# Performance work log

Measured on AMD Instinct MI355X. Metric: run time of the kernel, lower is better.

Reference implementation:

```python
import jax, jax.numpy as jnp
import numpy as np

B, N, C, H = 2, 2048, 1024, 16
D = C // H
EPS = 1e-5  # torch LayerNorm default


def layernorm(x, gamma, beta):
    mu = jnp.mean(x, axis=-1, keepdims=True)
    var = jnp.mean(jnp.square(x - mu), axis=-1, keepdims=True)
    return (x - mu) * jax.lax.rsqrt(var + EPS) * gamma + beta


def setup_inputs() -> dict:
    key = jax.random.key(0)
    ks = jax.random.split(key, 4)
    x = jax.random.normal(ks[0], (B, N, C), dtype=jnp.float32)
    w_qkv = jax.random.normal(ks[1], (3 * C, C), dtype=jnp.float32) * (C ** -0.5)
    w_proj = jax.random.normal(ks[2], (C, C), dtype=jnp.float32) * (C ** -0.5)
    return {
        "x": x,
        "w_qkv": w_qkv,
        "q_gamma": jnp.ones((C,), jnp.float32),
        "q_beta": jnp.zeros((C,), jnp.float32),
        "k_gamma": jnp.ones((C,), jnp.float32),
        "k_beta": jnp.zeros((C,), jnp.float32),
        "lpe_w": jnp.ones((C,), jnp.float32),
        "lpe_b": jnp.zeros((C,), jnp.float32),
        "w_proj": w_proj,
        "b_proj": jnp.zeros((C,), jnp.float32),
    }


def reference(x, w_qkv, q_gamma, q_beta, k_gamma, k_beta, lpe_w, lpe_b, w_proj, b_proj):
    b, n, c = x.shape
    scale = D ** -0.5
    qkv = jnp.einsum('bnc,fc->bnf', x, w_qkv)            # (B,N,3C)
    qkv = qkv.reshape(b, n, 3, H, D)
    q, k, v = qkv[:, :, 0], qkv[:, :, 1], qkv[:, :, 2]   # (B,N,H,D)
    # QK-norm: LayerNorm over flattened heads (dim C)
    q = layernorm(q.reshape(b, n, c), q_gamma, q_beta).reshape(b, n, H, D)
    k = layernorm(k.reshape(b, n, c), k_gamma, k_beta).reshape(b, n, H, D)
    # LPE: depthwise 1x1x1 conv == per-channel affine on v
    v_lpe = v.reshape(b, n, c) * lpe_w + lpe_b           # (B,N,C)
    # attention
    attn = jnp.einsum('bqhd,bkhd->bhqk', q * scale, k)   # (B,H,N,N)
    attn = jax.nn.softmax(attn, axis=-1)
    out = jnp.einsum('bhqk,bkhd->bqhd', attn, v).reshape(b, n, c)
    y = jnp.einsum('bnc,oc->bno', out + v_lpe, w_proj) + b_proj
    return y
```

## Files before the change

### kernel.cpp

```cpp
#include <hip/hip_runtime.h>
#include <stdint.h>

#define Bdim 2
#define Ndim 2048
#define Cdim 1024
#define Hdim 16
#define Ddim 64
#define Fdim 3072
#define Mdim 4096

typedef unsigned int  u32;
typedef unsigned short u16;
typedef float f32x4 __attribute__((ext_vector_type(4)));
typedef short s16x8 __attribute__((ext_vector_type(8)));
typedef unsigned short u16x4 __attribute__((ext_vector_type(4)));
typedef unsigned int u32x2 __attribute__((ext_vector_type(2)));

__device__ __forceinline__ u16 f2b(float f) {
  u32 u = __builtin_bit_cast(u32, f);
  u += 0x7FFFu + ((u >> 16) & 1u);
  return (u16)(u >> 16);
}
__device__ __forceinline__ float b2f(u16 h) {
  return __builtin_bit_cast(float, (u32)h << 16);
}
__device__ __forceinline__ u32 cvtpk(float a, float b) {
  u32 d;
  asm("v_cvt_pk_bf16_f32 %0, %1, %2" : "=v"(d) : "v"(a), "v"(b));
  return d;
}
__device__ __forceinline__ float rexp2(float x) { return __builtin_amdgcn_exp2f(x); }
__device__ __forceinline__ f32x4 mfma16(s16x8 a, s16x8 b, f32x4 c) {
  return __builtin_amdgcn_mfma_f32_16x16x32_bf16(a, b, c, 0, 0, 0);
}
__device__ __forceinline__ void gl_lds16(const void* g, void* l) {
  __builtin_amdgcn_global_load_lds(
      (const __attribute__((address_space(1))) void*)g,
      (__attribute__((address_space(3))) void*)l, 16, 0, 0);
}
__device__ __forceinline__ bool is_bf16(const void* qg) {
  return *(const u32*)qg == 0x3F803F80u;
}

__global__ __launch_bounds__(256)
void k_prep(const void* x, const void* wq, const void* wp,
            const void* g0, const void* g1, const void* g2, const void* g3,
            const void* g4, const void* g5, const void* g6,
            u16* xb, u16* wqb, u16* wpb, float* prm) {
  const int i = blockIdx.x * 256 + threadIdx.x;
  const bool isbf = is_bf16(g0);
  const void* src; u16* dst; int k;
  if (i < 1048576)      { src = x;  dst = xb;  k = i; }
  else if (i < 1835008) { src = wq; dst = wqb; k = i - 1048576; }
  else if (i < 2097152) { src = wp; dst = wpb; k = i - 1835008; }
  else {
    const int j = i - 2097152;
    if (j >= 1792) return;
    const int fi = j * 4;
    const int pi = fi >> 10, off = fi & 1023;
    const void* s = (pi == 0) ? g0 : (pi == 1) ? g1 : (pi == 2) ? g2
                  : (pi == 3) ? g3 : (pi == 4) ? g4 : (pi == 5) ? g5 : g6;
    float4 v;
    if (isbf) {
      u16x4 h = *(const u16x4*)((const u16*)s + off);
      v.x = b2f(h.x); v.y = b2f(h.y); v.z = b2f(h.z); v.w = b2f(h.w);
    } else {
      v = *(const float4*)((const float*)s + off);
    }
    *(float4*)(prm + fi) = v;
    return;
  }
  if (isbf) {
    ((u16x4*)dst)[k] = ((const u16x4*)src)[k];
  } else {
    float4 v = ((const float4*)src)[k];
    u16x4 o;
    o.x = f2b(v.x); o.y = f2b(v.y); o.z = f2b(v.z); o.w = f2b(v.w);
    ((u16x4*)dst)[k] = o;
  }
}

template <int EPI>
__global__ __launch_bounds__(256)
void k_gemm_bt(const u16* __restrict__ A, const u16* __restrict__ W,
               u16* __restrict__ Cb, void* __restrict__ Cout,
               u16* __restrict__ vTp,
               const float* __restrict__ bias, const void* __restrict__ qg,
               int Msz, int Nsz, int Ksz) {
  __shared__ __align__(16) char lds[32768];
  const int tid = threadIdx.x;
  const int lane = tid & 63;
  const int wm = (tid >> 6) >> 1, wn = (tid >> 6) & 1;
  const int g = lane >> 4, cl = lane & 15;
  const int nwg = gridDim.x * gridDim.y;
  const int lid = blockIdx.y * gridDim.x + blockIdx.x;
  const int cpx = nwg >> 3;
  const int swz = (lid & 7) * cpx + (lid >> 3);
  const int row0 = (swz / gridDim.x) * 128, col0 = (swz % gridDim.x) * 128;
  const int KT = Ksz >> 5;

  f32x4 acc[4][4] = {};

  auto stage = [&](int buf, int kt) {
    const int k0 = kt << 5;
#pragma unroll
    for (int iss = 0; iss < 2; ++iss) {
      const int t = iss * 256 + tid;
      const int r = t >> 2;
      const int ss = (t & 3) ^ ((r >> 1) & 3);
      gl_lds16(A + (size_t)(row0 + r) * Ksz + k0 + ss * 8, &lds[buf * 16384 + t * 16]);
      gl_lds16(W + (size_t)(col0 + r) * Ksz + k0 + ss * 8, &lds[buf * 16384 + 8192 + t * 16]);
    }
  };

  stage(0, 0);
  __syncthreads();
  int cur = 0;
  for (int kt = 0; kt < KT; ++kt) {
    if (kt + 1 < KT) stage(cur ^ 1, kt + 1);
    const char* Ab = &lds[cur * 16384];
    const char* Bb = &lds[cur * 16384 + 8192];
    s16x8 af[4], bfr[4];
#pragma unroll
    for (int mi = 0; mi < 4; ++mi) {
      const int r = wm * 64 + mi * 16 + cl;
      const int s = g ^ ((r >> 1) & 3);
      af[mi] = *(const s16x8*)(Ab + r * 64 + s * 16);
    }
#pragma unroll
    for (int nj = 0; nj < 4; ++nj) {
      const int r = wn * 64 + nj * 16 + cl;
      const int s = g ^ ((r >> 1) & 3);
      bfr[nj] = *(const s16x8*)(Bb + r * 64 + s * 16);
    }
#pragma unroll
    for (int mi = 0; mi < 4; ++mi)
#pragma unroll
      for (int nj = 0; nj < 4; ++nj)
        acc[mi][nj] = mfma16(af[mi], bfr[nj], acc[mi][nj]);
    __syncthreads();
    cur ^= 1;
  }

  const u32 oflag = (EPI == 1) ? (is_bf16(qg) ? 1u : 0u) : 0u;
#pragma unroll
  for (int mi = 0; mi < 4; ++mi)
#pragma unroll
    for (int nj = 0; nj < 4; ++nj) {
      const int m0 = row0 + wm * 64 + mi * 16 + g * 4;
      const int nbase = col0 + wn * 64 + nj * 16;
      const int n = nbase + cl;
      if (EPI == 2 && nbase >= 2048) {
        const int h = (nbase - 2048) >> 6;
        const int d = ((nbase - 2048) & 63) + cl;
        u16x4 pk;
#pragma unroll
        for (int r = 0; r < 4; ++r) pk[r] = f2b(acc[mi][nj][r]);
        *(u16x4*)(vTp + (size_t)h * (64 * 4096) + (size_t)d * 4096 + m0) = pk;
      } else {
#pragma unroll
        for (int r = 0; r < 4; ++r) {
          const int m = m0 + r;
          float v = acc[mi][nj][r];
          if (EPI == 2) {
            Cb[(size_t)m * Nsz + n] = f2b(v);
          } else {
            v += bias[n];
            if (oflag) ((u16*)Cout)[(size_t)m * Nsz + n] = f2b(v);
            else       ((float*)Cout)[(size_t)m * Nsz + n] = v;
          }
        }
      }
    }
}

__global__ __launch_bounds__(256)
void k_ln(u16* __restrict__ qkv, const float* __restrict__ prm) {
  const int m = blockIdx.x;
  const int tid = threadIdx.x;
  const int lane = tid & 63, wv = tid >> 6;
  __shared__ float red[2][4];
  u16* row = qkv + (size_t)m * Fdim;
#pragma unroll
  for (int seg = 0; seg < 2; ++seg) {
    u16* s = row + seg * 1024;
    u16x4 v = *(const u16x4*)(s + tid * 4);
    float x0 = b2f(v.x), x1 = b2f(v.y), x2 = b2f(v.z), x3 = b2f(v.w);
    float sum = x0 + x1 + x2 + x3;
    float ssq = x0 * x0 + x1 * x1 + x2 * x2 + x3 * x3;
#pragma unroll
    for (int off = 32; off >= 1; off >>= 1) {
      sum += __shfl_xor(sum, off);
      ssq += __shfl_xor(ssq, off);
    }
    if (lane == 0) { red[0][wv] = sum; red[1][wv] = ssq; }
    __syncthreads();
    const float ts = red[0][0] + red[0][1] + red[0][2] + red[0][3];
    const float tq = red[1][0] + red[1][1] + red[1][2] + red[1][3];
    __syncthreads();
    const float mu = ts * (1.0f / 1024.0f);
    const float var = tq * (1.0f / 1024.0f) - mu * mu;
    const float rstd = rsqrtf(var + 1e-5f);
    const float scl = (seg == 0) ? (0.125f * 1.4426950408889634f) : 1.0f;
    const float* gam = prm + seg * 2048;
    const float* bet = prm + seg * 2048 + 1024;
    const int c = tid * 4;
    u16x4 o;
    o.x = f2b(((x0 - mu) * rstd * gam[c + 0] + bet[c + 0]) * scl);
    o.y = f2b(((x1 - mu) * rstd * gam[c + 1] + bet[c + 1]) * scl);
    o.z = f2b(((x2 - mu) * rstd * gam[c + 2] + bet[c + 2]) * scl);
    o.w = f2b(((x3 - mu) * rstd * gam[c + 3] + bet[c + 3]) * scl);
    *(u16x4*)(s + tid * 4) = o;
  }
}

__global__ __launch_bounds__(256, 3)
void k_attn(const u16* __restrict__ qkv, const u16* __restrict__ vT,
            u16* __restrict__ pin, const float* __restrict__ prm) {
  const int bid = blockIdx.x;
  const int qt = (bid >> 3) & 15;
  const int bh = (bid & 7) * 4 + (bid >> 7);
  const int b = bh >> 4, h = bh & 15;
  const int tid = threadIdx.x, lane = tid & 63, w = tid >> 6;
  const int g = lane >> 4, cl = lane & 15;
  const int c7 = cl & 7;
  const int mrow0 = b * Ndim + qt * 128;
  const int NT = Ndim / 64;

  const u16* Qg  = qkv + (size_t)mrow0 * Fdim + h * 64;
  const u16* Kg  = qkv + (size_t)(b * Ndim) * Fdim + Cdim + h * 64;
  const u16* vTg = vT + (size_t)h * (64 * 4096) + b * Ndim;

  __shared__ __align__(16) char klds[2][8192];
  __shared__ __align__(16) char vlds[2][8192];
  __shared__ __align__(16) char plds[4][4096];

  s16x8 bq[2][2];
#pragma unroll
  for (int qb = 0; qb < 2; ++qb)
#pragma unroll
    for (int kc = 0; kc < 2; ++kc)
      bq[qb][kc] = *(const s16x8*)(Qg + (size_t)(w * 32 + qb * 16 + cl) * Fdim + kc * 32 + g * 8);

  f32x4 o[2][4] = {};
  float mr[2] = {-1e30f, -1e30f};
  float lr[2] = {0.f, 0.f};

  const char* akp0 = &klds[0][cl * 128 + (((0 + g) ^ c7) << 4)];
  const char* akp1 = &klds[0][cl * 128 + (((4 + g) ^ c7) << 4)];
  const char* avp0 = &vlds[0][cl * 128 + (((0 + g) ^ c7) << 4)];
  const char* avp1 = &vlds[0][cl * 128 + (((4 + g) ^ c7) << 4)];
  char* pwp[4];
#pragma unroll
  for (int nj = 0; nj < 4; ++nj)
    pwp[nj] = &plds[w][cl * 128 + ((nj * 32 + g * 8) ^ (c7 << 4))];
  const char* bpp0 = &plds[w][cl * 128 + ((0  + g * 16) ^ (c7 << 4))];
  const char* bpp1 = &plds[w][cl * 128 + ((64 + g * 16) ^ (c7 << 4))];

  const int r0 = tid >> 3;
  const int ss0 = ((tid & 7) ^ (r0 & 7)) * 8;
  const u16* kp = Kg + (size_t)r0 * Fdim + ss0;
  const u16* vp = vTg + (size_t)r0 * 4096 + ss0;
  char* kd = &klds[0][tid * 16];
  char* vd = &vlds[0][tid * 16];

  gl_lds16(kp, kd);
  gl_lds16(kp + (size_t)32 * Fdim, kd + 4096);
  gl_lds16(vp, vd);
  gl_lds16(vp + (size_t)32 * 4096, vd + 4096);
  kp += (size_t)64 * Fdim;
  vp += 64;

#define ATTN_TILE(BUF, PREFETCH)                                              \
  {                                                                           \
               \
    asm volatile("s_waitcnt vmcnt(2)" ::: "memory");                          \
    __builtin_amdgcn_s_barrier();                                             \
    __builtin_amdgcn_sched_barrier(0);                                        \
    if (PREFETCH) {                                                           \
      gl_lds16(kp, kd + ((BUF) ^ 1) * 8192);                                  \
      gl_lds16(kp + (size_t)32 * Fdim, kd + ((BUF) ^ 1) * 8192 + 4096);       \
      gl_lds16(vp, vd + ((BUF) ^ 1) * 8192);                                  \
      gl_lds16(vp + (size_t)32 * 4096, vd + ((BUF) ^ 1) * 8192 + 4096);       \
      kp += (size_t)64 * Fdim;                                                \
      vp += 64;                                                               \
    }                                                                         \
    s16x8 ak[4][2];                                                           \
    _Pragma("unroll") for (int nj = 0; nj < 4; ++nj) {                        \
      ak[nj][0] = *(const s16x8*)(akp0 + (BUF) * 8192 + nj * 2048);           \
      ak[nj][1] = *(const s16x8*)(akp1 + (BUF) * 8192 + nj * 2048);           \
    }                                                                         \
    _Pragma("unroll") for (int qb = 0; qb < 2; ++qb) {                        \
      f32x4 sv[4];                                                            \
      __builtin_amdgcn_s_setprio(1);                                          \
      _Pragma("unroll") for (int nj = 0; nj < 4; ++nj) {                      \
        f32x4 z = {0.f, 0.f, 0.f, 0.f};                                       \
        z = mfma16(ak[nj][0], bq[qb][0], z);                                  \
        z = mfma16(ak[nj][1], bq[qb][1], z);                                  \
        sv[nj] = z;                                                           \
      }                                                                       \
      __builtin_amdgcn_s_setprio(0);                                          \
      float a0 = fmaxf(fmaxf(sv[0][0], sv[0][1]), sv[0][2]);                  \
      float a1 = fmaxf(fmaxf(sv[0][3], sv[1][0]), sv[1][1]);                  \
      float a2 = fmaxf(fmaxf(sv[1][2], sv[1][3]), sv[2][0]);                  \
      float a3 = fmaxf(fmaxf(sv[2][1], sv[2][2]), sv[2][3]);                  \
      float a4 = fmaxf(fmaxf(sv[3][0], sv[3][1]), sv[3][2]);                  \
      float b0v = fmaxf(fmaxf(a0, a1), a2);                                   \
      float b1v = fmaxf(fmaxf(a3, a4), sv[3][3]);                             \
      float mx = fmaxf(b0v, b1v);                                             \
      if (!__all(mx <= mr[qb] + 7.0f)) {                                      \
        mx = fmaxf(mx, __shfl_xor(mx, 16));                                   \
        mx = fmaxf(mx, __shfl_xor(mx, 32));                                   \
        const float mn = fmaxf(mr[qb], mx);                                   \
        const float corr = rexp2(mr[qb] - mn);                                \
        mr[qb] = mn;                                                          \
        lr[qb] *= corr;                                                       \
        o[qb][0] *= corr; o[qb][1] *= corr;                                   \
        o[qb][2] *= corr; o[qb][3] *= corr;                                   \
      }                                                                       \
      const float mrq = mr[qb];                                               \
      float ssum = 0.f;                                                       \
      _Pragma("unroll") for (int nj = 0; nj < 4; ++nj) {                      \
        const float p0 = rexp2(sv[nj][0] - mrq), p1 = rexp2(sv[nj][1] - mrq); \
        const float p2 = rexp2(sv[nj][2] - mrq), p3 = rexp2(sv[nj][3] - mrq); \
        ssum += (p0 + p1) + (p2 + p3);                                        \
        u32x2 pk2;                                                            \
        pk2.x = cvtpk(p0, p1);                                                \
        pk2.y = cvtpk(p2, p3);                                                \
        *(u32x2*)(pwp[nj] + qb * 2048) = pk2;                                 \
      }                                                                       \
      lr[qb] += ssum;                                                         \
    }                                                                         \
           \
    if (PREFETCH) {                                                           \
      asm volatile("s_waitcnt vmcnt(4) lgkmcnt(0)" ::: "memory");             \
    } else {                                                                  \
      asm volatile("s_waitcnt vmcnt(0) lgkmcnt(0)" ::: "memory");             \
    }                                                                         \
    __builtin_amdgcn_s_barrier();                                             \
    __builtin_amdgcn_sched_barrier(0);                                        \
    s16x8 av[4][2];                                                           \
    _Pragma("unroll") for (int dc = 0; dc < 4; ++dc) {                        \
      av[dc][0] = *(const s16x8*)(avp0 + (BUF) * 8192 + dc * 2048);           \
      av[dc][1] = *(const s16x8*)(avp1 + (BUF) * 8192 + dc * 2048);           \
    }                                                                         \
    _Pragma("unroll") for (int qb = 0; qb < 2; ++qb) {                        \
      const s16x8 bp0 = *(const s16x8*)(bpp0 + qb * 2048);                    \
      const s16x8 bp1 = *(const s16x8*)(bpp1 + qb * 2048);                    \
      __builtin_amdgcn_s_setprio(1);                                          \
      _Pragma("unroll") for (int dc = 0; dc < 4; ++dc) {                      \
        o[qb][dc] = mfma16(av[dc][0], bp0, o[qb][dc]);                        \
        o[qb][dc] = mfma16(av[dc][1], bp1, o[qb][dc]);                        \
      }                                                                       \
      __builtin_amdgcn_s_setprio(0);                                          \
    }                                                                         \
  }

  for (int t = 0; t < NT; t += 2) {
    ATTN_TILE(0, true);
    ATTN_TILE(1, (t + 2 < NT));
  }
#undef ATTN_TILE

#pragma unroll
  for (int qb = 0; qb < 2; ++qb) {
    const int q = w * 32 + qb * 16 + cl;
    const int m = mrow0 + q;
    const int nseq = qt * 128 + q;
    float lt = lr[qb];
    lt += __shfl_xor(lt, 16);
    lt += __shfl_xor(lt, 32);
    const float inv = 1.0f / lt;
#pragma unroll
    for (int dc = 0; dc < 4; ++dc) {
      const int d0 = dc * 16 + g * 4;
      const int c = h * 64 + d0;
      const float4 lw = *(const float4*)(prm + 4096 + c);
      const float4 lb = *(const float4*)(prm + 5120 + c);
      float vr[4];
#pragma unroll
      for (int r = 0; r < 4; ++r) {
        const float vv = b2f(vTg[(size_t)(d0 + r) * 4096 + nseq]);
        vr[r] = o[qb][dc][r] * inv + vv * (&lw.x)[r] + (&lb.x)[r];
      }
      u32x2 ov;
      ov.x = cvtpk(vr[0], vr[1]);
      ov.y = cvtpk(vr[2], vr[3]);
      *(u32x2*)(pin + (size_t)m * Cdim + c) = ov;
    }
  }
}

extern "C" void kernel_launch(void* const* d_in, const int* in_sizes, int n_in,
                              void* d_out, int out_size, void* d_ws, size_t ws_size,
                              hipStream_t stream) {
  (void)in_sizes; (void)n_in; (void)out_size; (void)ws_size;
  char* ws = (char*)d_ws;
  float* prm    = (float*)(ws + 256);
  u16*   xb     = (u16*)(ws + 32768);
  u16*   wqkvb  = (u16*)(ws + 32768 + 8388608);
  u16*   wprojb = (u16*)(ws + 32768 + 8388608 + 6291456);
  u16*   qkv    = (u16*)(ws + 32768 + 8388608 + 6291456 + 2097152);
  u16*   vT     = (u16*)(ws + 32768 + 8388608 + 6291456 + 2097152 + 25165824);
  u16*   pin    = xb;

  k_prep<<<8199, 256, 0, stream>>>(d_in[0], d_in[1], d_in[8],
                                   d_in[2], d_in[3], d_in[4], d_in[5],
                                   d_in[6], d_in[7], d_in[9],
                                   xb, wqkvb, wprojb, prm);

  k_gemm_bt<2><<<dim3(Fdim / 128, Mdim / 128), 256, 0, stream>>>(
      xb, wqkvb, qkv, nullptr, vT, nullptr, nullptr, Mdim, Fdim, Cdim);

  k_ln<<<Mdim, 256, 0, stream>>>(qkv, prm);

  k_attn<<<dim3(512), 256, 0, stream>>>(qkv, vT, pin, prm);

  k_gemm_bt<1><<<dim3(Cdim / 128, Mdim / 128), 256, 0, stream>>>(
      pin, wprojb, nullptr, d_out, nullptr, prm + 6144, d_in[2], Mdim, Cdim, Cdim);
}
```

Before: 133.2 us.

## Use 128x64 tiles for output projection GEMM and batch QK MFMAs in attention

The output projection GEMM moves from a 128x128 tile kernel (256 workgroups) to a dedicated 128x64 tile kernel, which doubles the workgroup count to 512 so the 256 CUs are better filled. The QKV GEMM becomes its own non-templated kernel. In attention, the QK^T MFMAs for both query blocks are now issued together under raised priority before the softmax work, so more matrix ops can be in flight. The smaller tile reloads the A operand twice as often and lowers per-wave reuse, and holding both score blocks at once raises register pressure in the attention kernel.

```diff
diff --git a/kernel.cpp b/kernel.cpp
--- a/kernel.cpp
+++ b/kernel.cpp
@@ -80,13 +80,10 @@
   }
 }
 
-template <int EPI>
 __global__ __launch_bounds__(256)
-void k_gemm_bt(const u16* __restrict__ A, const u16* __restrict__ W,
-               u16* __restrict__ Cb, void* __restrict__ Cout,
-               u16* __restrict__ vTp,
-               const float* __restrict__ bias, const void* __restrict__ qg,
-               int Msz, int Nsz, int Ksz) {
+void k_gemm_qkv(const u16* __restrict__ A, const u16* __restrict__ W,
+                u16* __restrict__ Cb, u16* __restrict__ vTp,
+                int Msz, int Nsz, int Ksz) {
   __shared__ __align__(16) char lds[32768];
   const int tid = threadIdx.x;
   const int lane = tid & 63;
@@ -142,7 +139,6 @@
     cur ^= 1;
   }
 
-  const u32 oflag = (EPI == 1) ? (is_bf16(qg) ? 1u : 0u) : 0u;
 #pragma unroll
   for (int mi = 0; mi < 4; ++mi)
 #pragma unroll
@@ -150,7 +146,7 @@
       const int m0 = row0 + wm * 64 + mi * 16 + g * 4;
       const int nbase = col0 + wn * 64 + nj * 16;
       const int n = nbase + cl;
-      if (EPI == 2 && nbase >= 2048) {
+      if (nbase >= 2048) {
         const int h = (nbase - 2048) >> 6;
         const int d = ((nbase - 2048) & 63) + cl;
         u16x4 pk;
@@ -159,17 +155,87 @@
         *(u16x4*)(vTp + (size_t)h * (64 * 4096) + (size_t)d * 4096 + m0) = pk;
       } else {
 #pragma unroll
-        for (int r = 0; r < 4; ++r) {
-          const int m = m0 + r;
-          float v = acc[mi][nj][r];
-          if (EPI == 2) {
-            Cb[(size_t)m * Nsz + n] = f2b(v);
-          } else {
-            v += bias[n];
-            if (oflag) ((u16*)Cout)[(size_t)m * Nsz + n] = f2b(v);
-            else       ((float*)Cout)[(size_t)m * Nsz + n] = v;
-          }
-        }
+        for (int r = 0; r < 4; ++r)
+          Cb[(size_t)(m0 + r) * Nsz + n] = f2b(acc[mi][nj][r]);
+      }
+    }
+}
+
+__global__ __launch_bounds__(256)
+void k_gemm_n64(const u16* __restrict__ A, const u16* __restrict__ W,
+                void* __restrict__ Cout, const float* __restrict__ bias,
+                const void* __restrict__ qg) {
+  __shared__ __align__(16) char lds[24576];
+  const int tid = threadIdx.x;
+  const int lane = tid & 63;
+  const int w = tid >> 6;
+  const int g = lane >> 4, cl = lane & 15;
+  const int nwg = gridDim.x * gridDim.y;
+  const int lid = blockIdx.y * gridDim.x + blockIdx.x;
+  const int cpx = nwg >> 3;
+  const int swz = (lid & 7) * cpx + (lid >> 3);
+  const int row0 = (swz / gridDim.x) * 128, col0 = (swz % gridDim.x) * 64;
+  const int KT = Cdim >> 5;
+
+  f32x4 acc[2][4] = {};
+
+  auto stage = [&](int buf, int kt) {
+    const int k0 = kt << 5;
+#pragma unroll
+    for (int iss = 0; iss < 2; ++iss) {
+      const int t = iss * 256 + tid;
+      const int r = t >> 2;
+      const int ss = (t & 3) ^ ((r >> 1) & 3);
+      gl_lds16(A + (size_t)(row0 + r) * Cdim + k0 + ss * 8, &lds[buf * 12288 + t * 16]);
+    }
+    {
+      const int r = tid >> 2;
+      const int ss = (tid & 3) ^ ((r >> 1) & 3);
+      gl_lds16(W + (size_t)(col0 + r) * Cdim + k0 + ss * 8, &lds[buf * 12288 + 8192 + tid * 16]);
+    }
+  };
+
+  stage(0, 0);
+  __syncthreads();
+  int cur = 0;
+  for (int kt = 0; kt < KT; ++kt) {
+    if (kt + 1 < KT) stage(cur ^ 1, kt + 1);
+    const char* Ab = &lds[cur * 12288];
+    const char* Bb = &lds[cur * 12288 + 8192];
+    s16x8 af[2], bfr[4];
+#pragma unroll
+    for (int mi = 0; mi < 2; ++mi) {
+      const int r = w * 32 + mi * 16 + cl;
+      const int s = g ^ ((r >> 1) & 3);
+      af[mi] = *(const s16x8*)(Ab + r * 64 + s * 16);
+    }
+#pragma unroll
+    for (int nj = 0; nj < 4; ++nj) {
+      const int r = nj * 16 + cl;
+      const int s = g ^ ((r >> 1) & 3);
+      bfr[nj] = *(const s16x8*)(Bb + r * 64 + s * 16);
+    }
+#pragma unroll
+    for (int mi = 0; mi < 2; ++mi)
+#pragma unroll
+      for (int nj = 0; nj < 4; ++nj)
+        acc[mi][nj] = mfma16(af[mi], bfr[nj], acc[mi][nj]);
+    __syncthreads();
+    cur ^= 1;
+  }
+
+  const u32 oflag = is_bf16(qg) ? 1u : 0u;
+#pragma unroll
+  for (int mi = 0; mi < 2; ++mi)
+#pragma unroll
+    for (int nj = 0; nj < 4; ++nj) {
+      const int m0 = row0 + w * 32 + mi * 16 + g * 4;
+      const int n = col0 + nj * 16 + cl;
+#pragma unroll
+      for (int r = 0; r < 4; ++r) {
+        float v = acc[mi][nj][r] + bias[n];
+        if (oflag) ((u16*)Cout)[(size_t)(m0 + r) * Cdim + n] = f2b(v);
+        else       ((float*)Cout)[(size_t)(m0 + r) * Cdim + n] = v;
       }
     }
 }
@@ -290,23 +356,25 @@
       ak[nj][0] = *(const s16x8*)(akp0 + (BUF) * 8192 + nj * 2048);           \
       ak[nj][1] = *(const s16x8*)(akp1 + (BUF) * 8192 + nj * 2048);           \
     }                                                                         \
-    _Pragma("unroll") for (int qb = 0; qb < 2; ++qb) {                        \
-      f32x4 sv[4];                                                            \
-      __builtin_amdgcn_s_setprio(1);                                          \
+                       \
+    f32x4 sv[2][4];                                                           \
+    __builtin_amdgcn_s_setprio(1);                                            \
+    _Pragma("unroll") for (int qb = 0; qb < 2; ++qb)                          \
       _Pragma("unroll") for (int nj = 0; nj < 4; ++nj) {                      \
         f32x4 z = {0.f, 0.f, 0.f, 0.f};                                       \
         z = mfma16(ak[nj][0], bq[qb][0], z);                                  \
         z = mfma16(ak[nj][1], bq[qb][1], z);                                  \
-        sv[nj] = z;                                                           \
+        sv[qb][nj] = z;                                                       \
       }                                                                       \
-      __builtin_amdgcn_s_setprio(0);                                          \
-      float a0 = fmaxf(fmaxf(sv[0][0], sv[0][1]), sv[0][2]);                  \
-      float a1 = fmaxf(fmaxf(sv[0][3], sv[1][0]), sv[1][1]);                  \
-      float a2 = fmaxf(fmaxf(sv[1][2], sv[1][3]), sv[2][0]);                  \
-      float a3 = fmaxf(fmaxf(sv[2][1], sv[2][2]), sv[2][3]);                  \
-      float a4 = fmaxf(fmaxf(sv[3][0], sv[3][1]), sv[3][2]);                  \
+    __builtin_amdgcn_s_setprio(0);                                            \
+    _Pragma("unroll") for (int qb = 0; qb < 2; ++qb) {                        \
+      float a0 = fmaxf(fmaxf(sv[qb][0][0], sv[qb][0][1]), sv[qb][0][2]);      \
+      float a1 = fmaxf(fmaxf(sv[qb][0][3], sv[qb][1][0]), sv[qb][1][1]);      \
+      float a2 = fmaxf(fmaxf(sv[qb][1][2], sv[qb][1][3]), sv[qb][2][0]);      \
+      float a3 = fmaxf(fmaxf(sv[qb][2][1], sv[qb][2][2]), sv[qb][2][3]);      \
+      float a4 = fmaxf(fmaxf(sv[qb][3][0], sv[qb][3][1]), sv[qb][3][2]);      \
       float b0v = fmaxf(fmaxf(a0, a1), a2);                                   \
-      float b1v = fmaxf(fmaxf(a3, a4), sv[3][3]);                             \
+      float b1v = fmaxf(fmaxf(a3, a4), sv[qb][3][3]);                         \
       float mx = fmaxf(b0v, b1v);                                             \
       if (!__all(mx <= mr[qb] + 7.0f)) {                                      \
         mx = fmaxf(mx, __shfl_xor(mx, 16));                                   \
@@ -321,8 +389,10 @@
       const float mrq = mr[qb];                                               \
       float ssum = 0.f;                                                       \
       _Pragma("unroll") for (int nj = 0; nj < 4; ++nj) {                      \
-        const float p0 = rexp2(sv[nj][0] - mrq), p1 = rexp2(sv[nj][1] - mrq); \
-        const float p2 = rexp2(sv[nj][2] - mrq), p3 = rexp2(sv[nj][3] - mrq); \
+        const float p0 = rexp2(sv[qb][nj][0] - mrq);                          \
+        const float p1 = rexp2(sv[qb][nj][1] - mrq);                          \
+        const float p2 = rexp2(sv[qb][nj][2] - mrq);                          \
+        const float p3 = rexp2(sv[qb][nj][3] - mrq);                          \
         ssum += (p0 + p1) + (p2 + p3);                                        \
         u32x2 pk2;                                                            \
         pk2.x = cvtpk(p0, p1);                                                \
@@ -409,13 +479,13 @@
                                    d_in[6], d_in[7], d_in[9],
                                    xb, wqkvb, wprojb, prm);
 
-  k_gemm_bt<2><<<dim3(Fdim / 128, Mdim / 128), 256, 0, stream>>>(
-      xb, wqkvb, qkv, nullptr, vT, nullptr, nullptr, Mdim, Fdim, Cdim);
+  k_gemm_qkv<<<dim3(Fdim / 128, Mdim / 128), 256, 0, stream>>>(
+      xb, wqkvb, qkv, vT, Mdim, Fdim, Cdim);
 
   k_ln<<<Mdim, 256, 0, stream>>>(qkv, prm);
 
   k_attn<<<dim3(512), 256, 0, stream>>>(qkv, vT, pin, prm);
 
-  k_gemm_bt<1><<<dim3(Cdim / 128, Mdim / 128), 256, 0, stream>>>(
-      pin, wprojb, nullptr, d_out, nullptr, prm + 6144, d_in[2], Mdim, Cdim, Cdim);
-}
+  k_gemm_n64<<<dim3(Cdim / 64, Mdim / 128), 256, 0, stream>>>(
+      pin, wprojb, d_out, prm + 6144, d_in[2]);
+}
```

Result: faster. 130.5 us (-2.1%).
